# Kernel tuning notes

Hardware: AMD Instinct MI355X
Metric: run time of the kernel (lower is better)

Reference implementation:

```python
import jax, jax.numpy as jnp
import numpy as np

EPS = 1e-10
N_ITERS = 20
TEMP = 1.0


def sinkhorn(log_alpha, temp, n_iters):
    # incomplete Sinkhorn normalization over last two dims
    la = log_alpha / temp
    for _ in range(n_iters):
        la = la - jax.nn.logsumexp(la, axis=-2, keepdims=True)  # column norm
        la = la - jax.nn.logsumexp(la, axis=-1, keepdims=True)  # row norm
    return jnp.exp(la)


def setup_inputs() -> dict:
    key = jax.random.key(0)
    k1, k2, k3 = jax.random.split(key, 3)
    S, B, D, N = 4, 8, 1024, 1024  # samples, batch, feature rows, perm size
    x = jax.random.normal(k1, (B, D, N), dtype=jnp.float32)
    # kaiming_uniform_ default (a=sqrt(5)) -> bound = 1/sqrt(fan_in)
    bound = 1.0 / np.sqrt(N)
    log_alpha = jax.random.uniform(k2, (N, N), jnp.float32, -bound, bound)
    u = jax.random.uniform(k3, (S, B, N, N), jnp.float32)  # uniform draws for gumbel
    return {"x": x, "log_alpha": log_alpha, "u": u}


def reference(x, log_alpha, u):
    # gumbel noise: -log(eps - log(U + eps)) as in sample_gumbel
    gumbel = -jnp.log(EPS - jnp.log(u + EPS))
    log_alpha_noise = log_alpha + gumbel                  # (S,B,N,N)
    soft_perms = sinkhorn(log_alpha_noise, TEMP, N_ITERS)  # (S,B,N,N)
    # x.unsqueeze(0) @ soft_perms -> (S,B,D,N)
    return jnp.einsum('bdn,sbnm->sbdm', x, soft_perms)
```

## Files before the change

### kernel.cpp

```cpp
#include <hip/hip_runtime.h>

#define EPS 1e-10f
#define NITERS 20
#define NN (1024*1024)

typedef __attribute__((ext_vector_type(8))) short bf16x8;
typedef __attribute__((ext_vector_type(4))) float f32x4;

__device__ __forceinline__ unsigned short f2bf(float f) {
  unsigned int x = __builtin_bit_cast(unsigned int, f);
  x += 0x7fffu + ((x >> 16) & 1u);
  return (unsigned short)(x >> 16);
}
__device__ __forceinline__ float bf2f(short s) {
  return __builtin_bit_cast(float, ((unsigned int)(unsigned short)s) << 16);
}

__device__ __forceinline__ void pv_store2(float* p, float a, float b) {
  unsigned long long v = (unsigned long long)__builtin_bit_cast(unsigned int, a)
                       | ((unsigned long long)__builtin_bit_cast(unsigned int, b) << 32);
  __hip_atomic_store((unsigned long long*)p, v, __ATOMIC_RELAXED, __HIP_MEMORY_SCOPE_AGENT);
}
__device__ __forceinline__ float2 pv_load2(const float* p) {
  unsigned long long v = __hip_atomic_load((const unsigned long long*)p,
                                           __ATOMIC_RELAXED, __HIP_MEMORY_SCOPE_AGENT);
  float2 r;
  r.x = __builtin_bit_cast(float, (unsigned int)(v & 0xffffffffull));
  r.y = __builtin_bit_cast(float, (unsigned int)(v >> 32));
  return r;
}

__device__ __forceinline__ void mat_barrier(unsigned* c, unsigned target) {
  __syncthreads();
  if (threadIdx.x == 0) {
    __hip_atomic_fetch_add(c, 1u, __ATOMIC_RELAXED, __HIP_MEMORY_SCOPE_AGENT);
    while (__hip_atomic_load(c, __ATOMIC_RELAXED, __HIP_MEMORY_SCOPE_AGENT) < target) {
      __builtin_amdgcn_s_sleep(8);
    }
  }
  __syncthreads();
}

__global__ __launch_bounds__(512) void sinkhorn_coop(const float* __restrict__ u,
                                                     const float* __restrict__ la,
                                                     unsigned short* __restrict__ Kb,
                                                     float* __restrict__ pvA,
                                                     float* __restrict__ pvB,
                                                     unsigned short* __restrict__ Pt,
                                                     unsigned* __restrict__ cnt) {
  int bid = blockIdx.x;
  int tid = threadIdx.x;
  int l = tid & 63, w = tid >> 6;
  int mloc = bid & 15;
  int ch = bid >> 4;
  int r0 = ch << 6;

  __shared__ float smem[8][1024];
  __shared__ float v_lds[1024];
  __shared__ float u_lds[64];
  __shared__ unsigned short tile[64][66];

  for (int g = 0; g < 2; ++g) {
    int mat = g * 16 + mloc;
    const float* ub = u + (size_t)mat * NN;
    unsigned short* Ks = Kb + (size_t)mat * NN;
    float* pA = pvA + ((size_t)mat << 14);
    float* pB = pvB + ((size_t)mat << 14);
    unsigned* c = cnt + (size_t)mat * 1024;

    {
      float colacc[16];
#pragma unroll
      for (int k2 = 0; k2 < 16; ++k2) colacc[k2] = 0.f;
#pragma unroll 1
      for (int p = 0; p < 8; ++p) {
        int row = r0 + (p << 3) + w;
        const f32x4* u4 = (const f32x4*)(ub + (size_t)row * 1024 + l * 16);
        const f32x4* la4 = (const f32x4*)(la + (size_t)row * 1024 + l * 16);
        float kf[16];
#pragma unroll
        for (int q = 0; q < 4; ++q) {
          f32x4 uv = __builtin_nontemporal_load(u4 + q);
          f32x4 lv = __builtin_nontemporal_load(la4 + q);
#pragma unroll
          for (int e = 0; e < 4; ++e)
            kf[q * 4 + e] = expf(lv[e]) / (EPS - logf(uv[e] + EPS));
        }
        bf16x8 o0, o1;
#pragma unroll
        for (int j = 0; j < 8; ++j) {
          o0[j] = (short)f2bf(kf[j]);
          o1[j] = (short)f2bf(kf[8 + j]);
          colacc[j] += kf[j];
          colacc[8 + j] += kf[8 + j];
        }
        bf16x8* kp = (bf16x8*)(Ks + (size_t)row * 1024 + l * 16);
        kp[0] = o0; kp[1] = o1;
      }
#pragma unroll
      for (int k2 = 0; k2 < 16; ++k2) smem[w][l * 16 + k2] = colacc[k2];
      __syncthreads();
      if (tid < 256) {
        float4 s = make_float4(0.f, 0.f, 0.f, 0.f);
#pragma unroll
        for (int ww = 0; ww < 8; ++ww) {
          float4 a = *(float4*)&smem[ww][tid * 4];
          s.x += a.x; s.y += a.y; s.z += a.z; s.w += a.w;
        }
        float* slot = pA + (ch << 10);
        pv_store2(&slot[tid * 4], s.x, s.y);
        pv_store2(&slot[tid * 4 + 2], s.z, s.w);
      }
      mat_barrier(c, 16u);
    }

    const float* pin = pA;
    float* pout = pB;
#pragma unroll 1
    for (int t = 1; t < NITERS; ++t) {
      {
        float2 s = make_float2(0.f, 0.f);
#pragma unroll
        for (int cc = 0; cc < 16; ++cc) {
          float2 a = pv_load2(pin + (cc << 10) + 2 * tid);
          s.x += a.x; s.y += a.y;
        }
        v_lds[2 * tid] = 1.f / s.x;
        v_lds[2 * tid + 1] = 1.f / s.y;
      }
      __syncthreads();
      float vreg[16];
#pragma unroll
      for (int k2 = 0; k2 < 16; ++k2) vreg[k2] = v_lds[l * 16 + k2];

      float colacc[16];
#pragma unroll
      for (int k2 = 0; k2 < 16; ++k2) colacc[k2] = 0.f;
#pragma unroll 2
      for (int p = 0; p < 8; ++p) {
        int row = r0 + (p << 3) + w;
        const bf16x8* kp = (const bf16x8*)(Ks + (size_t)row * 1024 + l * 16);
        bf16x8 k0 = kp[0], k1 = kp[1];
        float kf[16];
#pragma unroll
        for (int j = 0; j < 8; ++j) { kf[j] = bf2f(k0[j]); kf[8 + j] = bf2f(k1[j]); }
        float dot = 0.f;
#pragma unroll
        for (int k2 = 0; k2 < 16; ++k2) dot += kf[k2] * vreg[k2];
#pragma unroll
        for (int m = 1; m < 64; m <<= 1) dot += __shfl_xor(dot, m, 64);
        float ui = 1.0f / dot;
#pragma unroll
        for (int k2 = 0; k2 < 16; ++k2) colacc[k2] += kf[k2] * ui;
      }
#pragma unroll
      for (int k2 = 0; k2 < 16; ++k2) smem[w][l * 16 + k2] = colacc[k2];
      __syncthreads();
      if (tid < 256) {
        float4 s = make_float4(0.f, 0.f, 0.f, 0.f);
#pragma unroll
        for (int ww = 0; ww < 8; ++ww) {
          float4 a = *(float4*)&smem[ww][tid * 4];
          s.x += a.x; s.y += a.y; s.z += a.z; s.w += a.w;
        }
        float* slot = pout + (ch << 10);
        pv_store2(&slot[tid * 4], s.x, s.y);
        pv_store2(&slot[tid * 4 + 2], s.z, s.w);
      }
      mat_barrier(c, 16u * (unsigned)(t + 1));
      float* tp = pout; pout = (float*)pin; pin = tp;
    }

    {
      float2 s = make_float2(0.f, 0.f);
#pragma unroll
      for (int cc = 0; cc < 16; ++cc) {
        float2 a = pv_load2(pin + (cc << 10) + 2 * tid);
        s.x += a.x; s.y += a.y;
      }
      v_lds[2 * tid] = 1.f / s.x;
      v_lds[2 * tid + 1] = 1.f / s.y;
    }
    __syncthreads();
    {
      float vreg[16];
#pragma unroll
      for (int k2 = 0; k2 < 16; ++k2) vreg[k2] = v_lds[l * 16 + k2];
#pragma unroll 1
      for (int p = 0; p < 8; ++p) {
        int row = r0 + (p << 3) + w;
        const bf16x8* kp = (const bf16x8*)(Ks + (size_t)row * 1024 + l * 16);
        bf16x8 k0 = kp[0], k1 = kp[1];
        float dot = 0.f;
#pragma unroll
        for (int j = 0; j < 8; ++j) dot += bf2f(k0[j]) * vreg[j] + bf2f(k1[j]) * vreg[8 + j];
#pragma unroll
        for (int m = 1; m < 64; m <<= 1) dot += __shfl_xor(dot, m, 64);
        if (l == 0) u_lds[(p << 3) + w] = 1.0f / dot;
      }
    }
    __syncthreads();
    {
      unsigned short* Pb = Pt + (size_t)mat * NN;
      int cc = tid & 63, r8 = tid >> 6;
#pragma unroll 1
      for (int mt = 0; mt < 16; ++mt) {
        int m0 = mt << 6;
#pragma unroll
        for (int p = 0; p < 8; ++p) {
          int rr = (p << 3) + r8;
          float val = bf2f((short)Ks[(size_t)(r0 + rr) * 1024 + m0 + cc]) * u_lds[rr] * v_lds[m0 + cc];
          tile[rr][cc] = f2bf(val);
        }
        __syncthreads();
#pragma unroll
        for (int p = 0; p < 8; ++p) {
          int rr = (p << 3) + r8;
          Pb[(size_t)(m0 + rr) * 1024 + r0 + cc] = tile[cc][rr];
        }
        __syncthreads();
      }
    }
  }
}

__global__ __launch_bounds__(256) void cvt_x(const float4* __restrict__ x4,
                                             unsigned short* __restrict__ xb) {
  int gid = blockIdx.x * 256 + threadIdx.x;
  float4 v = x4[gid];
  ushort4 o;
  o.x = f2bf(v.x); o.y = f2bf(v.y); o.z = f2bf(v.z); o.w = f2bf(v.w);
  *(ushort4*)&xb[(size_t)gid * 4] = o;
}

__global__ __launch_bounds__(256) void gemm_bf16(const unsigned short* __restrict__ xb,
                                                 const unsigned short* __restrict__ Pt,
                                                 float* __restrict__ out) {
  int bid = blockIdx.x;
  int lid = (bid & 7) * 256 + (bid >> 3);
  int sb = lid >> 6;
  int tm = (lid >> 3) & 7;
  int tn = lid & 7;
  int b = sb & 7;
  const unsigned short* A = xb + (size_t)b * NN;
  const unsigned short* Bt = Pt + (size_t)sb * NN;
  float* C = out + (size_t)sb * NN;

  __shared__ unsigned short lA[128 * 32];
  __shared__ unsigned short lB[128 * 32];

  int tid = threadIdx.x;
  int lane = tid & 63;
  int w = tid >> 6;
  int wm = (w >> 1) << 6;
  int wn = (w & 1) << 6;

  f32x4 acc[4][4] = {};

  int lr = tid >> 2;
  int lk = (tid & 3) << 3;
  const unsigned short* gA0 = A + (size_t)(tm * 128 + lr) * 1024 + lk;
  const unsigned short* gB0 = Bt + (size_t)(tn * 128 + lr) * 1024 + lk;

  for (int k0 = 0; k0 < 1024; k0 += 32) {
    __builtin_amdgcn_global_load_lds((const __attribute__((address_space(1))) void*)(gA0 + k0),
                                     (__attribute__((address_space(3))) void*)&lA[tid * 8], 16, 0, 0);
    __builtin_amdgcn_global_load_lds((const __attribute__((address_space(1))) void*)(gA0 + 64 * 1024 + k0),
                                     (__attribute__((address_space(3))) void*)&lA[2048 + tid * 8], 16, 0, 0);
    __builtin_amdgcn_global_load_lds((const __attribute__((address_space(1))) void*)(gB0 + k0),
                                     (__attribute__((address_space(3))) void*)&lB[tid * 8], 16, 0, 0);
    __builtin_amdgcn_global_load_lds((const __attribute__((address_space(1))) void*)(gB0 + 64 * 1024 + k0),
                                     (__attribute__((address_space(3))) void*)&lB[2048 + tid * 8], 16, 0, 0);
    __syncthreads();

    int kg = (lane >> 4) << 3;
    int rr = lane & 15;
    bf16x8 af[4], bfr[4];
#pragma unroll
    for (int mt = 0; mt < 4; ++mt)
      af[mt] = *(const bf16x8*)&lA[(wm + mt * 16 + rr) * 32 + kg];
#pragma unroll
    for (int nt = 0; nt < 4; ++nt)
      bfr[nt] = *(const bf16x8*)&lB[(wn + nt * 16 + rr) * 32 + kg];
#pragma unroll
    for (int mt = 0; mt < 4; ++mt)
#pragma unroll
      for (int nt = 0; nt < 4; ++nt)
        acc[mt][nt] = __builtin_amdgcn_mfma_f32_16x16x32_bf16(af[mt], bfr[nt], acc[mt][nt], 0, 0, 0);
    __syncthreads();
  }

  int col0 = lane & 15;
  int row0 = (lane >> 4) << 2;
#pragma unroll
  for (int mt = 0; mt < 4; ++mt) {
#pragma unroll
    for (int nt = 0; nt < 4; ++nt) {
      int row = tm * 128 + wm + mt * 16 + row0;
      int col = tn * 128 + wn + nt * 16 + col0;
#pragma unroll
      for (int r = 0; r < 4; ++r)
        C[(size_t)(row + r) * 1024 + col] = acc[mt][nt][r];
    }
  }
}

extern "C" void kernel_launch(void* const* d_in, const int* in_sizes, int n_in,
                              void* d_out, int out_size, void* d_ws, size_t ws_size,
                              hipStream_t stream) {
  (void)in_sizes; (void)n_in; (void)out_size;
  const float* x  = (const float*)d_in[0];
  const float* la = (const float*)d_in[1];
  const float* u  = (const float*)d_in[2];
  float* out = (float*)d_out;

  char* ws = (char*)d_ws;
  unsigned short* Kb = (unsigned short*)(ws);
  unsigned short* Pt = (unsigned short*)(ws + 67108864);
  unsigned short* xb = (unsigned short*)(ws + 134217728);
  float* pvA         = (float*)(ws + 150994944);
  float* pvB         = (float*)(ws + 153092096);
  unsigned* cnt      = (unsigned*)(ws + 155189248);
  if (ws_size < 155320320) return;

  hipMemsetAsync((void*)cnt, 0, 131072, stream);
  cvt_x<<<8192, 256, 0, stream>>>((const float4*)x, xb);

  void* args[] = {(void*)&u, (void*)&la, (void*)&Kb, (void*)&pvA,
                  (void*)&pvB, (void*)&Pt, (void*)&cnt};
  hipLaunchCooperativeKernel((void*)sinkhorn_coop, dim3(256), dim3(512),
                             args, 0, stream);

  gemm_bf16<<<2048, 256, 0, stream>>>(xb, Pt, out);
}
```

Before: 526.9 us.

## Keep per-block Sinkhorn K tile resident in LDS across iterations

Adds a new Sinkhorn kernel in which each block holds its 64x1024 bf16 slice of the kernel matrix K in shared memory (128KB) for all iterations, instead of re-reading K from global memory every iteration. The 32 matrices are now handled in two cooperative launches of 256 blocks with 256 threads each. Row and column scaling vectors still go through global memory with atomic-flag barriers. This removes the repeated global traffic on K, but relies on large LDS per block, which limits occupancy to one block per CU, and adds a second cooperative launch.

```diff
diff --git a/kernel.cpp b/kernel.cpp
--- a/kernel.cpp
+++ b/kernel.cpp
@@ -41,13 +41,212 @@
   __syncthreads();
 }
 
-__global__ __launch_bounds__(512) void sinkhorn_coop(const float* __restrict__ u,
-                                                     const float* __restrict__ la,
-                                                     unsigned short* __restrict__ Kb,
-                                                     float* __restrict__ pvA,
-                                                     float* __restrict__ pvB,
-                                                     unsigned short* __restrict__ Pt,
-                                                     unsigned* __restrict__ cnt) {
+__global__ __launch_bounds__(256) void sinkhorn_lds(const float* __restrict__ u,
+                                                    const float* __restrict__ la,
+                                                    float* __restrict__ pvA,
+                                                    float* __restrict__ pvB,
+                                                    unsigned short* __restrict__ Pt,
+                                                    unsigned* __restrict__ cnt,
+                                                    int g) {
+  int bid = blockIdx.x;
+  int tid = threadIdx.x;
+  int l = tid & 63, w = tid >> 6;
+  int mat = g * 16 + (bid & 15);
+  int ch = bid >> 4;
+  int r0 = ch << 6;
+
+  __shared__ unsigned short Kl[64 * 1024];
+  __shared__ __align__(16) float v_lds[1024];
+  __shared__ __align__(16) float sacc[1024];
+  __shared__ float u_lds[64];
+  __shared__ unsigned short tile[64][66];
+
+  const float* ub = u + (size_t)mat * NN;
+  float* pA = pvA + ((size_t)mat << 14);
+  float* pB = pvB + ((size_t)mat << 14);
+  unsigned* c = cnt + (size_t)mat * 1024;
+
+  {
+    float colacc[16];
+#pragma unroll
+    for (int k2 = 0; k2 < 16; ++k2) colacc[k2] = 0.f;
+#pragma unroll 1
+    for (int p = 0; p < 16; ++p) {
+      int lr = (p << 2) + w;
+      int row = r0 + lr;
+      const f32x4* u4 = (const f32x4*)(ub + (size_t)row * 1024 + l * 16);
+      const f32x4* la4 = (const f32x4*)(la + (size_t)row * 1024 + l * 16);
+      float kf[16];
+#pragma unroll
+      for (int q = 0; q < 4; ++q) {
+        f32x4 uv = __builtin_nontemporal_load(u4 + q);
+        f32x4 lv = __builtin_nontemporal_load(la4 + q);
+#pragma unroll
+        for (int e = 0; e < 4; ++e)
+          kf[q * 4 + e] = expf(lv[e]) / (EPS - logf(uv[e] + EPS));
+      }
+      bf16x8 o0, o1;
+#pragma unroll
+      for (int j = 0; j < 8; ++j) {
+        o0[j] = (short)f2bf(kf[j]);
+        o1[j] = (short)f2bf(kf[8 + j]);
+        colacc[j] += kf[j];
+        colacc[8 + j] += kf[8 + j];
+      }
+      bf16x8* kp = (bf16x8*)&Kl[lr * 1024 + l * 16];
+      kp[0] = o0; kp[1] = o1;
+    }
+    if (w == 0) {
+#pragma unroll
+      for (int k2 = 0; k2 < 16; ++k2) sacc[l * 16 + k2] = colacc[k2];
+    }
+    __syncthreads();
+#pragma unroll 1
+    for (int ww = 1; ww < 4; ++ww) {
+      if (w == ww) {
+#pragma unroll
+        for (int k2 = 0; k2 < 16; ++k2) sacc[l * 16 + k2] += colacc[k2];
+      }
+      __syncthreads();
+    }
+    float4 s = *(float4*)&sacc[tid * 4];
+    float* slot = pA + (ch << 10);
+    pv_store2(&slot[tid * 4], s.x, s.y);
+    pv_store2(&slot[tid * 4 + 2], s.z, s.w);
+    mat_barrier(c, 16u);
+  }
+
+  const float* pin = pA;
+  float* pout = pB;
+#pragma unroll 1
+  for (int t = 1; t < NITERS; ++t) {
+    {
+      float s0 = 0.f, s1 = 0.f, s2 = 0.f, s3 = 0.f;
+#pragma unroll
+      for (int cc = 0; cc < 16; ++cc) {
+        float2 a = pv_load2(pin + (cc << 10) + 4 * tid);
+        float2 b = pv_load2(pin + (cc << 10) + 4 * tid + 2);
+        s0 += a.x; s1 += a.y; s2 += b.x; s3 += b.y;
+      }
+      v_lds[4 * tid + 0] = 1.f / s0;
+      v_lds[4 * tid + 1] = 1.f / s1;
+      v_lds[4 * tid + 2] = 1.f / s2;
+      v_lds[4 * tid + 3] = 1.f / s3;
+    }
+    __syncthreads();
+    float vreg[16];
+#pragma unroll
+    for (int k2 = 0; k2 < 16; ++k2) vreg[k2] = v_lds[l * 16 + k2];
+
+    float colacc[16];
+#pragma unroll
+    for (int k2 = 0; k2 < 16; ++k2) colacc[k2] = 0.f;
+#pragma unroll 2
+    for (int p = 0; p < 16; ++p) {
+      int lr = (p << 2) + w;
+      const bf16x8* kp = (const bf16x8*)&Kl[lr * 1024 + l * 16];
+      bf16x8 k0 = kp[0], k1 = kp[1];
+      float kf[16];
+#pragma unroll
+      for (int j = 0; j < 8; ++j) { kf[j] = bf2f(k0[j]); kf[8 + j] = bf2f(k1[j]); }
+      float d0 = 0.f, d1 = 0.f, d2 = 0.f, d3 = 0.f;
+#pragma unroll
+      for (int k2 = 0; k2 < 4; ++k2) {
+        d0 += kf[k2] * vreg[k2];
+        d1 += kf[4 + k2] * vreg[4 + k2];
+        d2 += kf[8 + k2] * vreg[8 + k2];
+        d3 += kf[12 + k2] * vreg[12 + k2];
+      }
+      float dot = (d0 + d1) + (d2 + d3);
+#pragma unroll
+      for (int m = 1; m < 64; m <<= 1) dot += __shfl_xor(dot, m, 64);
+      float ui = 1.0f / dot;
+#pragma unroll
+      for (int k2 = 0; k2 < 16; ++k2) colacc[k2] += kf[k2] * ui;
+    }
+    if (w == 0) {
+#pragma unroll
+      for (int k2 = 0; k2 < 16; ++k2) sacc[l * 16 + k2] = colacc[k2];
+    }
+    __syncthreads();
+#pragma unroll 1
+    for (int ww = 1; ww < 4; ++ww) {
+      if (w == ww) {
+#pragma unroll
+        for (int k2 = 0; k2 < 16; ++k2) sacc[l * 16 + k2] += colacc[k2];
+      }
+      __syncthreads();
+    }
+    float4 s = *(float4*)&sacc[tid * 4];
+    float* slot = pout + (ch << 10);
+    pv_store2(&slot[tid * 4], s.x, s.y);
+    pv_store2(&slot[tid * 4 + 2], s.z, s.w);
+    mat_barrier(c, 16u * (unsigned)(t + 1));
+    float* tp = pout; pout = (float*)pin; pin = tp;
+  }
+
+  {
+    float s0 = 0.f, s1 = 0.f, s2 = 0.f, s3 = 0.f;
+#pragma unroll
+    for (int cc = 0; cc < 16; ++cc) {
+      float2 a = pv_load2(pin + (cc << 10) + 4 * tid);
+      float2 b = pv_load2(pin + (cc << 10) + 4 * tid + 2);
+      s0 += a.x; s1 += a.y; s2 += b.x; s3 += b.y;
+    }
+    v_lds[4 * tid + 0] = 1.f / s0;
+    v_lds[4 * tid + 1] = 1.f / s1;
+    v_lds[4 * tid + 2] = 1.f / s2;
+    v_lds[4 * tid + 3] = 1.f / s3;
+  }
+  __syncthreads();
+  {
+    float vreg[16];
+#pragma unroll
+    for (int k2 = 0; k2 < 16; ++k2) vreg[k2] = v_lds[l * 16 + k2];
+#pragma unroll 1
+    for (int p = 0; p < 16; ++p) {
+      int lr = (p << 2) + w;
+      const bf16x8* kp = (const bf16x8*)&Kl[lr * 1024 + l * 16];
+      bf16x8 k0 = kp[0], k1 = kp[1];
+      float dot = 0.f;
+#pragma unroll
+      for (int j = 0; j < 8; ++j) dot += bf2f(k0[j]) * vreg[j] + bf2f(k1[j]) * vreg[8 + j];
+#pragma unroll
+      for (int m = 1; m < 64; m <<= 1) dot += __shfl_xor(dot, m, 64);
+      if (l == 0) u_lds[lr] = 1.0f / dot;
+    }
+  }
+  __syncthreads();
+  {
+    unsigned short* Pb = Pt + (size_t)mat * NN;
+    int cc = tid & 63, r4 = tid >> 6;
+#pragma unroll 1
+    for (int mt = 0; mt < 16; ++mt) {
+      int m0 = mt << 6;
+#pragma unroll
+      for (int p = 0; p < 16; ++p) {
+        int rr = (p << 2) + r4;
+        float val = bf2f((short)Kl[rr * 1024 + m0 + cc]) * u_lds[rr] * v_lds[m0 + cc];
+        tile[rr][cc] = f2bf(val);
+      }
+      __syncthreads();
+#pragma unroll
+      for (int p = 0; p < 16; ++p) {
+        int rr = (p << 2) + r4;
+        Pb[(size_t)(m0 + rr) * 1024 + r0 + cc] = tile[cc][rr];
+      }
+      __syncthreads();
+    }
+  }
+}
+
+__global__ __launch_bounds__(512) void sinkhorn_coop_g(const float* __restrict__ u,
+                                                       const float* __restrict__ la,
+                                                       unsigned short* __restrict__ Kb,
+                                                       float* __restrict__ pvA,
+                                                       float* __restrict__ pvB,
+                                                       unsigned short* __restrict__ Pt,
+                                                       unsigned* __restrict__ cnt) {
   int bid = blockIdx.x;
   int tid = threadIdx.x;
   int l = tid & 63, w = tid >> 6;
@@ -326,10 +525,22 @@
   hipMemsetAsync((void*)cnt, 0, 131072, stream);
   cvt_x<<<8192, 256, 0, stream>>>((const float4*)x, xb);
 
-  void* args[] = {(void*)&u, (void*)&la, (void*)&Kb, (void*)&pvA,
-                  (void*)&pvB, (void*)&Pt, (void*)&cnt};
-  hipLaunchCooperativeKernel((void*)sinkhorn_coop, dim3(256), dim3(512),
-                             args, 0, stream);
+  int maxb = 0;
+  hipError_t qrc = hipOccupancyMaxActiveBlocksPerMultiprocessor(
+      &maxb, (const void*)sinkhorn_lds, 256, 0);
+  if (qrc == hipSuccess && maxb >= 1) {
+    for (int g = 0; g < 2; ++g) {
+      void* args[] = {(void*)&u, (void*)&la, (void*)&pvA, (void*)&pvB,
+                      (void*)&Pt, (void*)&cnt, (void*)&g};
+      hipLaunchCooperativeKernel((void*)sinkhorn_lds, dim3(256), dim3(256),
+                                 args, 0, stream);
+    }
+  } else {
+    void* args[] = {(void*)&u, (void*)&la, (void*)&Kb, (void*)&pvA,
+                    (void*)&pvB, (void*)&Pt, (void*)&cnt};
+    hipLaunchCooperativeKernel((void*)sinkhorn_coop_g, dim3(256), dim3(512),
+                               args, 0, stream);
+  }
 
   gemm_bf16<<<2048, 256, 0, stream>>>(xb, Pt, out);
 }
```

New measurement: 566.3 us. 1.07x slower.
